# Performance work log

Measured on AMD Instinct MI355X. Metric: run time of the kernel, lower is better.

The kernel has to match this reference:

```python
import jax, jax.numpy as jnp
import numpy as np

B, L, H, G = 16, 1024, 1024, 128


def setup_inputs() -> dict:
    key = jax.random.key(0)
    ks = jax.random.split(key, 6)
    s = 0.02
    return {
        "events": jax.random.normal(ks[0], (B, L, H), jnp.float32),
        "contexts": jax.random.normal(ks[1], (B, L - 1, H), jnp.float32),
        "Wzm": jax.random.normal(ks[2], (2 * H, G), jnp.float32) * s,
        "bzm": jnp.zeros((G,), jnp.float32),
        "Wzv": jax.random.normal(ks[3], (2 * H, G), jnp.float32) * s,
        "bzv": jnp.zeros((G,), jnp.float32),
        "Wqm": jax.random.normal(ks[4], (3 * H, G), jnp.float32) * s,
        "bqm": jnp.zeros((G,), jnp.float32),
        "Wqv": jax.random.normal(ks[5], (3 * H, G), jnp.float32) * s,
        "bqv": jnp.zeros((G,), jnp.float32),
    }


def reference(events, contexts, Wzm, bzm, Wzv, bzv, Wqm, bqm, Wqv, bqv):
    # adjacent event pairs: [B, L-1, 2H]
    ep = jnp.concatenate([events[:, :-1, :], events[:, 1:, :]], axis=-1)
    z_mean = ep @ Wzm + bzm          # [B, L-1, G]
    z_log_var = ep @ Wzv + bzv
    ce = jnp.concatenate([ep, contexts], axis=-1)  # [B, L-1, 3H]
    q_z_mean = ce @ Wqm + bqm
    q_z_log_var = ce @ Wqv + bqv
    # closed-form KL(p || q) for diagonal Gaussians, summed over G per (b, pair)
    kl = 0.5 * jnp.sum(
        q_z_log_var - z_log_var
        + (jnp.exp(z_log_var) + (z_mean - q_z_mean) ** 2) * jnp.exp(-q_z_log_var)
        - 1.0,
        axis=-1,
    )  # [B, L-1]
    kl_loss = jnp.mean(kl).reshape(1)  # sum over (b, pair) / (B * (L-1))
    return (z_mean, z_log_var, q_z_mean, q_z_log_var, kl_loss)
```

## Files before the change

### kernel.cpp

```cpp
#include <hip/hip_runtime.h>
#include <stdint.h>

typedef unsigned char u8;
typedef unsigned short u16;
typedef __attribute__((ext_vector_type(8))) short short8;
typedef __attribute__((ext_vector_type(4))) float f32x4;
typedef __attribute__((ext_vector_type(2))) uint32_t u32x2;

#define B_      16
#define L_      1024
#define H_      1024
#define G_      128
#define M_TOT   16368
#define K_TOT   3072
#define OUT_SEG 2095104
#define KL_IDX  (4*OUT_SEG)
#define KL_BLOCKS 2046
#define WSCALE  128.0f
#define WINV    0.0078125f

#define WS_WT_OFF    0
#define WS_BIAS_OFF  1572864
#define WS_PART_OFF  1574912

__device__ inline void gload16(const void* g, void* l) {
    __builtin_amdgcn_global_load_lds(
        (const __attribute__((address_space(1))) void*)g,
        (__attribute__((address_space(3))) void*)l, 16, 0, 0);
}

__device__ inline uint32_t pk4fp8(float f0, float f1, float f2, float f3) {
    uint32_t w = __builtin_amdgcn_cvt_pk_fp8_f32(f0, f1, 0, 0);
    w = __builtin_amdgcn_cvt_pk_fp8_f32(f2, f3, w, 1);
    return w;
}

__global__ __launch_bounds__(256) void prep_kernel(
    const float* __restrict__ Wzm, const float* __restrict__ bzm,
    const float* __restrict__ Wzv, const float* __restrict__ bzv,
    const float* __restrict__ Wqm, const float* __restrict__ bqm,
    const float* __restrict__ Wqv, const float* __restrict__ bqv,
    u8* __restrict__ wt, float* __restrict__ bias)
{
    const int ng = blockIdx.x >> 2;
    const int kq = blockIdx.x & 3;
    const int n0 = ng * 8;
    const float* W; const float* bsrc; int g0; int kmax;
    if (n0 < 128)      { W = Wzm; bsrc = bzm; g0 = n0;       kmax = 2048; }
    else if (n0 < 256) { W = Wzv; bsrc = bzv; g0 = n0 - 128; kmax = 2048; }
    else if (n0 < 384) { W = Wqm; bsrc = bqm; g0 = n0 - 256; kmax = 3072; }
    else               { W = Wqv; bsrc = bqv; g0 = n0 - 384; kmax = 3072; }
    const int tid = threadIdx.x;
    if (kq == 0 && tid < 8) bias[n0 + tid] = bsrc[g0 + tid];

    __shared__ float lt[8][260];
    const int go = tid & 7;
    const int kk = tid >> 3;
    const int nn = tid >> 5;
    const int kc = (tid & 31) * 8;

    for (int i = 0; i < 3; ++i) {
        int kbase = kq * 768 + i * 256;
        __syncthreads();
        #pragma unroll
        for (int kk2 = 0; kk2 < 8; ++kk2) {
            int k = kbase + kk2 * 32 + kk;
            float v = (k < kmax) ? W[(size_t)k * G_ + g0 + go] : 0.0f;
            lt[go][kk2 * 32 + kk] = v;
        }
        __syncthreads();
        uint32_t u0 = pk4fp8(lt[nn][kc + 0] * WSCALE, lt[nn][kc + 1] * WSCALE,
                             lt[nn][kc + 2] * WSCALE, lt[nn][kc + 3] * WSCALE);
        uint32_t u1 = pk4fp8(lt[nn][kc + 4] * WSCALE, lt[nn][kc + 5] * WSCALE,
                             lt[nn][kc + 6] * WSCALE, lt[nn][kc + 7] * WSCALE);
        *(u32x2*)&wt[(size_t)(n0 + nn) * K_TOT + kbase + kc] = (u32x2){u0, u1};
    }
}

__global__ __launch_bounds__(512, 2) void gemm_kernel(
    const float* __restrict__ events, const float* __restrict__ contexts,
    const u8* __restrict__ wt, const float* __restrict__ bias,
    float* __restrict__ out)
{
    __shared__ u8 Ab[2][128 * 64];
    __shared__ u8 Bs[2][128 * 64];

    const int tid = threadIdx.x;
    const int bid = blockIdx.x;
    const int xx  = bid & 7;
    const int jj  = bid >> 3;
    const int nb  = jj & 3;
    const int mp  = (jj >> 2) * 8 + xx;
    const int m0  = mp * 128;

    const int lane = tid & 63;
    const int w    = tid >> 6;
    const int wm   = (w >> 2) * 64;
    const int wn   = (w & 3) * 32;
    const int lr   = lane & 15;
    const int kg   = lane >> 4;

    const int r = tid >> 2;
    const int q = tid & 3;
    int m = m0 + r; if (m > M_TOT - 1) m = M_TOT - 1;
    int bb = m / 1023;
    int tt = m - bb * 1023;
    const float* paE = events   + ((size_t)(bb * L_ + tt)) * H_;
    const float* paC = contexts + ((size_t)(bb * (L_ - 1) + tt)) * H_;
    int aw[4];
    #pragma unroll
    for (int j = 0; j < 4; ++j)
        aw[j] = r * 64 + (((j ^ ((r >> 1) & 3))) << 4) + q * 4;

    const int bv   = tid >> 2;
    const int bc   = tid & 3;
    const int bcs  = bc ^ ((bv >> 1) & 3);
    const u8* bS = wt + (size_t)(nb * 128 + bv) * K_TOT + bcs * 16;

    int aoff[4][2], boff[2][2];
    #pragma unroll
    for (int i = 0; i < 4; ++i) {
        int row = wm + i * 16 + lr;
        #pragma unroll
        for (int ks = 0; ks < 2; ++ks) {
            int c16 = ks * 2 + (kg >> 1);
            aoff[i][ks] = row * 64 + ((c16 ^ ((row >> 1) & 3)) << 4) + (kg & 1) * 8;
        }
    }
    #pragma unroll
    for (int j = 0; j < 2; ++j) {
        int nn = wn + j * 16 + lr;
        #pragma unroll
        for (int ks = 0; ks < 2; ++ks) {
            int c16 = ks * 2 + (kg >> 1);
            boff[j][ks] = nn * 64 + ((c16 ^ ((nn >> 1) & 3)) << 4) + (kg & 1) * 8;
        }
    }

    f32x4 acc[4][2];
    #pragma unroll
    for (int i = 0; i < 4; ++i)
        #pragma unroll
        for (int j = 0; j < 2; ++j)
            acc[i][j] = (f32x4){0.f, 0.f, 0.f, 0.f};

    auto stageB = [&](int buf, int kt) {
        gload16(bS + kt * 64, &Bs[buf][tid * 16]);
    };
    auto compute = [&](int buf) {
        #pragma unroll
        for (int ks = 0; ks < 2; ++ks) {
            long a[4], bf[2];
            #pragma unroll
            for (int i = 0; i < 4; ++i)
                a[i] = *(const long*)&Ab[buf][aoff[i][ks]];
            #pragma unroll
            for (int j = 0; j < 2; ++j)
                bf[j] = *(const long*)&Bs[buf][boff[j][ks]];
            __builtin_amdgcn_s_setprio(1);
            #pragma unroll
            for (int i = 0; i < 4; ++i)
                #pragma unroll
                for (int j = 0; j < 2; ++j)
                    acc[i][j] = __builtin_amdgcn_mfma_f32_16x16x32_fp8_fp8(
                        a[i], bf[j], acc[i][j], 0, 0, 0);
            __builtin_amdgcn_s_setprio(0);
        }
    };

    f32x4 P0, P1, P2, P3;
    f32x4 Q0, Q1, Q2, Q3;

#define LOADA(p, KT)                                                           \
    {                                                                          \
        int k0_ = (KT) * 64;                                                   \
        int rg_ = (KT) >> 4;                                                   \
        int kq_ = (k0_ & 1023) + q * 4;                                        \
        const float* s_ = (rg_ == 0) ? paE : (rg_ == 1 ? (paE + H_) : paC);    \
        s_ += kq_;                                                             \
        p##0 = *(const f32x4*)(s_ +  0);                                       \
        p##1 = *(const f32x4*)(s_ + 16);                                       \
        p##2 = *(const f32x4*)(s_ + 32);                                       \
        p##3 = *(const f32x4*)(s_ + 48);                                       \
    }
#define CVT1(p, J, BUF)                                                        \
    {                                                                          \
        uint32_t w_ = pk4fp8(p##J[0], p##J[1], p##J[2], p##J[3]);              \
        *(uint32_t*)&Ab[BUF][aw[J]] = w_;                                      \
    }
#define CVTW(p, BUF)  CVT1(p, 0, BUF) CVT1(p, 1, BUF) CVT1(p, 2, BUF) CVT1(p, 3, BUF)

#define WAITV(N)                                                               \
    asm volatile("s_waitcnt vmcnt(" #N ")" ::: "memory");                      \
    __builtin_amdgcn_sched_barrier(0);
#define LGKM0                                                                  \
    asm volatile("s_waitcnt lgkmcnt(0)" ::: "memory");                         \
    __builtin_amdgcn_sched_barrier(0);
#define BAR __builtin_amdgcn_s_barrier()

    LOADA(P, 0);
    stageB(0, 0);
    WAITV(1);
    CVTW(P, 0);
    LOADA(Q, 1);
    LGKM0;

    for (int t = 0; t < 46; t += 2) {
        LOADA(P, t + 2);
        stageB(1, t + 1);
        WAITV(5); BAR;
        compute(0);
        CVTW(Q, 1);
        LGKM0; BAR;
        LOADA(Q, t + 3);
        stageB(0, t + 2);
        WAITV(5); BAR;
        compute(1);
        CVTW(P, 0);
        LGKM0; BAR;
    }
    stageB(1, 47);
    WAITV(1); BAR;
    compute(0);
    CVTW(Q, 1);
    LGKM0; BAR;
    WAITV(0); BAR;
    compute(1);

#undef LOADA
#undef CVT1
#undef CVTW
#undef WAITV
#undef LGKM0
#undef BAR

    const float* bptr = bias + nb * 128;
    float* obase = out + (size_t)nb * OUT_SEG;
    #pragma unroll
    for (int i = 0; i < 4; ++i) {
        int mloc = wm + i * 16 + kg * 4;
        #pragma unroll
        for (int j = 0; j < 2; ++j) {
            int g = wn + j * 16 + lr;
            float bv2 = bptr[g];
            #pragma unroll
            for (int rr = 0; rr < 4; ++rr) {
                int mo = m0 + mloc + rr;
                if (mo < M_TOT)
                    obase[(size_t)mo * G_ + g] = acc[i][j][rr] * WINV + bv2;
            }
        }
    }
}

__global__ __launch_bounds__(256) void kl_kernel(const float* __restrict__ out,
                                                 float* __restrict__ partial)
{
    int row  = blockIdx.x * 8 + (threadIdx.x >> 5);
    int col  = (threadIdx.x & 31) * 4;
    const float* zm  = out;
    const float* zlv = out + OUT_SEG;
    const float* qm  = out + (size_t)2 * OUT_SEG;
    const float* qlv = out + (size_t)3 * OUT_SEG;
    size_t base = (size_t)row * G_ + col;
    f32x4 a = *(const f32x4*)&zm[base];
    f32x4 b = *(const f32x4*)&zlv[base];
    f32x4 c = *(const f32x4*)&qm[base];
    f32x4 d = *(const f32x4*)&qlv[base];
    float s = 0.f;
    #pragma unroll
    for (int e = 0; e < 4; ++e) {
        float diff = a[e] - c[e];
        s += d[e] - b[e] + (__expf(b[e]) + diff * diff) * __expf(-d[e]) - 1.0f;
    }
    #pragma unroll
    for (int off = 32; off > 0; off >>= 1)
        s += __shfl_down(s, off);
    __shared__ float pw[4];
    int wid  = threadIdx.x >> 6;
    int lane = threadIdx.x & 63;
    if (lane == 0) pw[wid] = s;
    __syncthreads();
    if (threadIdx.x == 0)
        partial[blockIdx.x] = pw[0] + pw[1] + pw[2] + pw[3];
}

__global__ __launch_bounds__(256) void kl_final(const float* __restrict__ partial,
                                                float* __restrict__ out)
{
    float s = 0.f;
    for (int i = threadIdx.x; i < KL_BLOCKS; i += 256) s += partial[i];
    #pragma unroll
    for (int off = 32; off > 0; off >>= 1)
        s += __shfl_down(s, off);
    __shared__ float pw[4];
    int wid = threadIdx.x >> 6;
    int lane = threadIdx.x & 63;
    if (lane == 0) pw[wid] = s;
    __syncthreads();
    if (threadIdx.x == 0)
        out[KL_IDX] = 0.5f * (pw[0] + pw[1] + pw[2] + pw[3]) / (float)M_TOT;
}

extern "C" void kernel_launch(void* const* d_in, const int* in_sizes, int n_in,
                              void* d_out, int out_size, void* d_ws, size_t ws_size,
                              hipStream_t stream)
{
    const float* events   = (const float*)d_in[0];
    const float* contexts = (const float*)d_in[1];
    const float* Wzm = (const float*)d_in[2];
    const float* bzm = (const float*)d_in[3];
    const float* Wzv = (const float*)d_in[4];
    const float* bzv = (const float*)d_in[5];
    const float* Wqm = (const float*)d_in[6];
    const float* bqm = (const float*)d_in[7];
    const float* Wqv = (const float*)d_in[8];
    const float* bqv = (const float*)d_in[9];
    float* out = (float*)d_out;

    u8*    wt      = (u8*)((char*)d_ws + WS_WT_OFF);
    float* bias    = (float*)((char*)d_ws + WS_BIAS_OFF);
    float* partial = (float*)((char*)d_ws + WS_PART_OFF);

    prep_kernel<<<256, 256, 0, stream>>>(Wzm, bzm, Wzv, bzv, Wqm, bqm, Wqv, bqv,
                                         wt, bias);
    gemm_kernel<<<512, 512, 0, stream>>>(events, contexts, wt, bias, out);
    kl_kernel<<<KL_BLOCKS, 256, 0, stream>>>(out, partial);
    kl_final<<<1, 256, 0, stream>>>(partial, out);
}
```

Measured before the change: 90.48 us.

## Fuse KL reduction into GEMM epilogue by interleaving output column groups

Each GEMM block now computes 32 columns from each of the four output heads instead of 128 columns of one head. This is done by remapping which weight rows it loads. After writing its tile, the block re-reads the four matching slices (served from cache) and computes per-block KL partial sums, so the separate kl_kernel launch and its full pass over the outputs go away. The cost is a global write-then-read within the block, which relies on the barrier making the stores visible, plus narrower 32-column store segments per head.

```diff
diff --git a/kernel.cpp b/kernel.cpp
--- a/kernel.cpp
+++ b/kernel.cpp
@@ -3,7 +3,6 @@
 
 typedef unsigned char u8;
 typedef unsigned short u16;
-typedef __attribute__((ext_vector_type(8))) short short8;
 typedef __attribute__((ext_vector_type(4))) float f32x4;
 typedef __attribute__((ext_vector_type(2))) uint32_t u32x2;
 
@@ -15,7 +14,7 @@
 #define K_TOT   3072
 #define OUT_SEG 2095104
 #define KL_IDX  (4*OUT_SEG)
-#define KL_BLOCKS 2046
+#define KL_PARTS 512
 #define WSCALE  128.0f
 #define WINV    0.0078125f
 
@@ -80,7 +79,7 @@
 __global__ __launch_bounds__(512, 2) void gemm_kernel(
     const float* __restrict__ events, const float* __restrict__ contexts,
     const u8* __restrict__ wt, const float* __restrict__ bias,
-    float* __restrict__ out)
+    float* __restrict__ out, float* __restrict__ partial)
 {
     __shared__ u8 Ab[2][128 * 64];
     __shared__ u8 Bs[2][128 * 64];
@@ -89,7 +88,7 @@
     const int bid = blockIdx.x;
     const int xx  = bid & 7;
     const int jj  = bid >> 3;
-    const int nb  = jj & 3;
+    const int nbg = jj & 3;
     const int mp  = (jj >> 2) * 8 + xx;
     const int m0  = mp * 128;
 
@@ -115,7 +114,8 @@
     const int bv   = tid >> 2;
     const int bc   = tid & 3;
     const int bcs  = bc ^ ((bv >> 1) & 3);
-    const u8* bS = wt + (size_t)(nb * 128 + bv) * K_TOT + bcs * 16;
+    const int bwr  = (bv >> 5) * 128 + nbg * 32 + (bv & 31);
+    const u8* bS = wt + (size_t)bwr * K_TOT + bcs * 16;
 
     int aoff[4][2], boff[2][2];
     #pragma unroll
@@ -227,69 +227,77 @@
     WAITV(0); BAR;
     compute(1);
 
+    #pragma unroll
+    for (int i = 0; i < 4; ++i) {
+        int mloc = wm + i * 16 + kg * 4;
+        #pragma unroll
+        for (int j = 0; j < 2; ++j) {
+            int lcol = wn + j * 16 + lr;
+            int seg  = lcol >> 5;
+            int gc   = nbg * 32 + (lcol & 31);
+            float bv2 = bias[seg * 128 + gc];
+            float* ob = out + (size_t)seg * OUT_SEG + gc;
+            #pragma unroll
+            for (int rr = 0; rr < 4; ++rr) {
+                int mo = m0 + mloc + rr;
+                if (mo < M_TOT)
+                    ob[(size_t)mo * G_] = acc[i][j][rr] * WINV + bv2;
+            }
+        }
+    }
+
+    WAITV(0); BAR;
+    float s = 0.f;
+    {
+        int mo = m0 + r;
+        if (mo < M_TOT) {
+            size_t base = (size_t)mo * G_ + nbg * 32 + q * 8;
+            const float* p0 = out + base;
+            const float* p1 = out + OUT_SEG + base;
+            const float* p2 = out + (size_t)2 * OUT_SEG + base;
+            const float* p3 = out + (size_t)3 * OUT_SEG + base;
+            #pragma unroll
+            for (int h = 0; h < 2; ++h) {
+                f32x4 av = *(const f32x4*)(p0 + h * 4);
+                f32x4 bv = *(const f32x4*)(p1 + h * 4);
+                f32x4 cv = *(const f32x4*)(p2 + h * 4);
+                f32x4 dv = *(const f32x4*)(p3 + h * 4);
+                #pragma unroll
+                for (int e = 0; e < 4; ++e) {
+                    float diff = av[e] - cv[e];
+                    s += dv[e] - bv[e]
+                       + (__expf(bv[e]) + diff * diff) * __expf(-dv[e]) - 1.0f;
+                }
+            }
+        }
+    }
+    #pragma unroll
+    for (int off = 32; off > 0; off >>= 1)
+        s += __shfl_down(s, off);
+    __shared__ float pw[8];
+    if (lane == 0) pw[w] = s;
+    BAR;
+    LGKM0;
+    if (tid == 0) {
+        float t2 = 0.f;
+        #pragma unroll
+        for (int i = 0; i < 8; ++i) t2 += pw[i];
+        partial[bid] = t2;
+    }
+
 #undef LOADA
 #undef CVT1
 #undef CVTW
 #undef WAITV
 #undef LGKM0
 #undef BAR
-
-    const float* bptr = bias + nb * 128;
-    float* obase = out + (size_t)nb * OUT_SEG;
-    #pragma unroll
-    for (int i = 0; i < 4; ++i) {
-        int mloc = wm + i * 16 + kg * 4;
-        #pragma unroll
-        for (int j = 0; j < 2; ++j) {
-            int g = wn + j * 16 + lr;
-            float bv2 = bptr[g];
-            #pragma unroll
-            for (int rr = 0; rr < 4; ++rr) {
-                int mo = m0 + mloc + rr;
-                if (mo < M_TOT)
-                    obase[(size_t)mo * G_ + g] = acc[i][j][rr] * WINV + bv2;
-            }
-        }
-    }
-}
-
-__global__ __launch_bounds__(256) void kl_kernel(const float* __restrict__ out,
-                                                 float* __restrict__ partial)
-{
-    int row  = blockIdx.x * 8 + (threadIdx.x >> 5);
-    int col  = (threadIdx.x & 31) * 4;
-    const float* zm  = out;
-    const float* zlv = out + OUT_SEG;
-    const float* qm  = out + (size_t)2 * OUT_SEG;
-    const float* qlv = out + (size_t)3 * OUT_SEG;
-    size_t base = (size_t)row * G_ + col;
-    f32x4 a = *(const f32x4*)&zm[base];
-    f32x4 b = *(const f32x4*)&zlv[base];
-    f32x4 c = *(const f32x4*)&qm[base];
-    f32x4 d = *(const f32x4*)&qlv[base];
-    float s = 0.f;
-    #pragma unroll
-    for (int e = 0; e < 4; ++e) {
-        float diff = a[e] - c[e];
-        s += d[e] - b[e] + (__expf(b[e]) + diff * diff) * __expf(-d[e]) - 1.0f;
-    }
-    #pragma unroll
-    for (int off = 32; off > 0; off >>= 1)
-        s += __shfl_down(s, off);
-    __shared__ float pw[4];
-    int wid  = threadIdx.x >> 6;
-    int lane = threadIdx.x & 63;
-    if (lane == 0) pw[wid] = s;
-    __syncthreads();
-    if (threadIdx.x == 0)
-        partial[blockIdx.x] = pw[0] + pw[1] + pw[2] + pw[3];
 }
 
 __global__ __launch_bounds__(256) void kl_final(const float* __restrict__ partial,
                                                 float* __restrict__ out)
 {
     float s = 0.f;
-    for (int i = threadIdx.x; i < KL_BLOCKS; i += 256) s += partial[i];
+    for (int i = threadIdx.x; i < KL_PARTS; i += 256) s += partial[i];
     #pragma unroll
     for (int off = 32; off > 0; off >>= 1)
         s += __shfl_down(s, off);
@@ -324,7 +332,6 @@
 
     prep_kernel<<<256, 256, 0, stream>>>(Wzm, bzm, Wzv, bzv, Wqm, bqm, Wqv, bqv,
                                          wt, bias);
-    gemm_kernel<<<512, 512, 0, stream>>>(events, contexts, wt, bias, out);
-    kl_kernel<<<KL_BLOCKS, 256, 0, stream>>>(out, partial);
+    gemm_kernel<<<512, 512, 0, stream>>>(events, contexts, wt, bias, out, partial);
     kl_final<<<1, 256, 0, stream>>>(partial, out);
 }
```

Measured after the change: 86.60 us. 1.04x faster.
